# Optimization experiments

Measured on AMD Instinct MI355X. Metric: run time of the kernel, lower is better.

The kernel has to match this reference:

```python
import jax, jax.numpy as jnp
import numpy as np
from jax import lax

EPS = 1e-6
NUM_BANDS = 128


def setup_inputs() -> dict:
    key = jax.random.key(0)
    kx, = jax.random.split(key, 1)
    B, C, F, T = 32, 1, NUM_BANDS, 6000
    x = jax.random.uniform(kx, (B, C, F, T), dtype=jnp.float32)  # nonneg spectrogram energies
    # parameters per band, initialized as in PCEN.__init__ (s=0.025, alpha=delta=r=1.0)
    log_s = jnp.full((F,), np.log(0.025), dtype=jnp.float32)
    log_alpha = jnp.zeros((F,), dtype=jnp.float32)
    log_delta = jnp.zeros((F,), dtype=jnp.float32)
    log_r = jnp.zeros((F,), dtype=jnp.float32)
    return {"x": x, "log_s": log_s, "log_alpha": log_alpha,
            "log_delta": log_delta, "log_r": log_r}


def _pcen(x, log_s, log_alpha, log_delta, log_r):
    # x: (B, C, bands, T)
    s = jnp.exp(log_s)  # (bands,)
    xt = jnp.moveaxis(x, -1, 0)  # (T, B, C, bands) time-major for the scan
    init = xt[0]  # init_smoother_from_data=True -> M_0 = X_0

    def step(m, xf):
        m_new = (1.0 - s) * m + s * xf
        return m_new, m_new

    _, ms = lax.scan(step, init, xt[1:])  # (T-1, B, C, bands)
    smoother = jnp.concatenate([init[None], ms], axis=0)  # (T, B, C, bands)
    smoother = jnp.moveaxis(smoother, 0, -1)  # (B, C, bands, T)

    alpha = jnp.exp(log_alpha)[:, None]  # (bands, 1)
    delta = jnp.exp(log_delta)[:, None]
    r = jnp.exp(log_r)[:, None]
    # (eps + M)^(-alpha) computed stably: exp(-alpha * (log eps + log1p(M/eps)))
    gain = jnp.exp(-alpha * (jnp.log(EPS) + jnp.log1p(smoother / EPS)))
    return (x * gain + delta) ** r - delta ** r


def reference(x, log_s, log_alpha, log_delta, log_r):
    return _pcen(x, log_s, log_alpha, log_delta, log_r)
```

## Files before the change

kernel.cpp:

```cpp
#include <hip/hip_runtime.h>

#define TLEN    6000
#define NV4     1500
#define CH_V4   512
#define SUB_V4  64
#define NSUB    8
#define EPS     1e-6f
#define LN_EPS  (-13.815511f)
#define INV_EPS 1e6f

__device__ __forceinline__ float pcen_full(float xv, float M, float alpha,
                                           float delta, float r, float deltar) {
    float gain = __expf(-alpha * (LN_EPS + __logf(fmaf(M, INV_EPS, 1.0f))));
    return __powf(fmaf(xv, gain, delta), r) - deltar;
}

__device__ __forceinline__ float ipow6(float b, int e) {
    float r = 1.0f;
    #pragma unroll
    for (int i = 0; i < 6; ++i) {
        if (e & 1) r *= b;
        b *= b;
        e >>= 1;
    }
    return r;
}

template<bool PARTIAL>
__device__ __forceinline__ float chunk_compute(
    const float4 (&q)[NSUB], const int cb, const int lane, const bool finit,
    const float s, const float oms, const float oms4, const float Apow4,
    const float A256, const bool triv,
    const float la, const float ld, const float lr,
    float Mc, float4* __restrict__ ob)
{
    float S[NSUB];
    #pragma unroll
    for (int j = 0; j < NSUB; ++j) {
        const float c0 = (finit && j == 0 && lane == 0) ? 1.0f : s;
        float b = c0 * q[j].x;
        b = fmaf(oms, b, s * q[j].y);
        b = fmaf(oms, b, s * q[j].z);
        b = fmaf(oms, b, s * q[j].w);
        S[j] = b;
    }

    float w = oms4;
    #pragma unroll
    for (int off = 1; off < 64; off <<= 1) {
        #pragma unroll
        for (int j = 0; j < NSUB; ++j) {
            const float Sp = __shfl_up(S[j], off, 64);
            if (lane >= off) S[j] = fmaf(w, Sp, S[j]);
        }
        w *= w;
    }

    float T[NSUB];
    #pragma unroll
    for (int j = 0; j < NSUB; ++j) T[j] = __shfl(S[j], 63, 64);
    float P[NSUB + 1];
    P[0] = Mc;
    #pragma unroll
    for (int j = 0; j < NSUB; ++j) P[j + 1] = fmaf(A256, P[j], T[j]);

    if (triv) {
        #pragma unroll
        for (int j = 0; j < NSUB; ++j) {
            const int vi = cb + SUB_V4 * j + lane;
            const float Se = __shfl_up(S[j], 1, 64);
            const float Be = (lane == 0) ? 0.0f : Se;
            float m = fmaf(Apow4, P[j], Be);
            if (!PARTIAL || vi < NV4) {
                const float c0 = (finit && j == 0 && lane == 0) ? 1.0f : s;
                float4 o;
                m = fmaf(oms, m, c0 * q[j].x); o.x = q[j].x * __builtin_amdgcn_rcpf(m + EPS);
                m = fmaf(oms, m, s  * q[j].y); o.y = q[j].y * __builtin_amdgcn_rcpf(m + EPS);
                m = fmaf(oms, m, s  * q[j].z); o.z = q[j].z * __builtin_amdgcn_rcpf(m + EPS);
                m = fmaf(oms, m, s  * q[j].w); o.w = q[j].w * __builtin_amdgcn_rcpf(m + EPS);
                ob[vi] = o;
            }
        }
    } else {
        const float alpha  = __expf(la);
        const float delta  = __expf(ld);
        const float r      = __expf(lr);
        const float deltar = __powf(delta, lr == 0.0f ? 1.0f : r);
        #pragma unroll
        for (int j = 0; j < NSUB; ++j) {
            const int vi = cb + SUB_V4 * j + lane;
            const float Se = __shfl_up(S[j], 1, 64);
            const float Be = (lane == 0) ? 0.0f : Se;
            float m = fmaf(Apow4, P[j], Be);
            if (!PARTIAL || vi < NV4) {
                const float c0 = (finit && j == 0 && lane == 0) ? 1.0f : s;
                float4 o;
                m = fmaf(oms, m, c0 * q[j].x); o.x = pcen_full(q[j].x, m, alpha, delta, r, deltar);
                m = fmaf(oms, m, s  * q[j].y); o.y = pcen_full(q[j].y, m, alpha, delta, r, deltar);
                m = fmaf(oms, m, s  * q[j].z); o.z = pcen_full(q[j].z, m, alpha, delta, r, deltar);
                m = fmaf(oms, m, s  * q[j].w); o.w = pcen_full(q[j].w, m, alpha, delta, r, deltar);
                ob[vi] = o;
            }
        }
    }
    return P[NSUB];
}

__global__ __launch_bounds__(256)
__attribute__((amdgpu_waves_per_eu(4, 4)))
void pcen_kernel(
    const float* __restrict__ x,
    const float* __restrict__ log_s,
    const float* __restrict__ log_alpha,
    const float* __restrict__ log_delta,
    const float* __restrict__ log_r,
    float* __restrict__ out,
    int num_series, int F)
{
    const int g    = (int)((blockIdx.x * blockDim.x + threadIdx.x) >> 6);
    const int lane = (int)(threadIdx.x & 63);
    if (g >= num_series) return;
    const int f = g % F;

    const float la = log_alpha[f], ld = log_delta[f], lr = log_r[f];
    const bool  triv = (la == 0.0f) && (ld == 0.0f) && (lr == 0.0f);

    const float s    = __expf(log_s[f]);
    const float oms  = 1.0f - s;
    const float oms2 = oms * oms;
    const float oms4 = oms2 * oms2;

    float A256 = oms4;
    #pragma unroll
    for (int i = 0; i < 6; ++i) A256 *= A256;

    const float Apow4 = ipow6(oms4, lane);

    const float4* __restrict__ xb = (const float4*)(x + (size_t)g * TLEN);
    float4* __restrict__ ob       = (float4*)(out + (size_t)g * TLEN);

    float4 bufA[NSUB], bufB[NSUB];

    #pragma unroll
    for (int j = 0; j < NSUB; ++j) bufA[j] = xb[SUB_V4 * j + lane];
    #pragma unroll
    for (int j = 0; j < NSUB; ++j) bufB[j] = xb[CH_V4 + SUB_V4 * j + lane];

    float Mc = 0.0f;

    Mc = chunk_compute<false>(bufA, 0, lane, true,
                              s, oms, oms4, Apow4, A256, triv, la, ld, lr, Mc, ob);

    #pragma unroll
    for (int j = 0; j < NSUB; ++j) {
        const int vi = 2 * CH_V4 + SUB_V4 * j + lane;
        bufA[j] = (vi < NV4) ? xb[vi] : make_float4(0.f, 0.f, 0.f, 0.f);
    }

    Mc = chunk_compute<false>(bufB, CH_V4, lane, false,
                              s, oms, oms4, Apow4, A256, triv, la, ld, lr, Mc, ob);

    chunk_compute<true>(bufA, 2 * CH_V4, lane, false,
                        s, oms, oms4, Apow4, A256, triv, la, ld, lr, Mc, ob);
}

extern "C" void kernel_launch(void* const* d_in, const int* in_sizes, int n_in,
                              void* d_out, int out_size, void* d_ws, size_t ws_size,
                              hipStream_t stream) {
    const float* x         = (const float*)d_in[0];
    const float* log_s     = (const float*)d_in[1];
    const float* log_alpha = (const float*)d_in[2];
    const float* log_delta = (const float*)d_in[3];
    const float* log_r     = (const float*)d_in[4];
    float* out             = (float*)d_out;

    const int F = in_sizes[1];
    const int num_series = in_sizes[0] / TLEN;
    const int num_waves  = num_series;
    const int num_threads = num_waves * 64;
    const int grid = (num_threads + 255) / 256;

    pcen_kernel<<<grid, 256, 0, stream>>>(x, log_s, log_alpha, log_delta, log_r,
                                          out, num_series, F);
}
```

Before: 207.1 us.

## Split each series across two waves with warm-up carry-in and reload inputs

Each time series is now handled by two waves, one per half of the sequence. The second half computes its starting smoother state itself. When the decay factor is negligible it uses a short 256-vector warm-up window before the half boundary; otherwise it replays the whole first half. This doubles the number of waves for more parallelism and latency hiding. In exchange it adds redundant reads, and it reloads x from memory in the output pass instead of keeping it in registers, which cuts register pressure. The warm-up shortcut is an approximation based on how fast the recurrence decays.

```diff
diff --git a/kernel.cpp b/kernel.cpp
--- a/kernel.cpp
+++ b/kernel.cpp
@@ -2,9 +2,10 @@
 
 #define TLEN    6000
 #define NV4     1500
-#define CH_V4   512
 #define SUB_V4  64
-#define NSUB    8
+#define NSUB    12
+#define H0_V4   768
+#define WARM_V4 256
 #define EPS     1e-6f
 #define LN_EPS  (-13.815511f)
 #define INV_EPS 1e6f
@@ -26,89 +27,7 @@
     return r;
 }
 
-template<bool PARTIAL>
-__device__ __forceinline__ float chunk_compute(
-    const float4 (&q)[NSUB], const int cb, const int lane, const bool finit,
-    const float s, const float oms, const float oms4, const float Apow4,
-    const float A256, const bool triv,
-    const float la, const float ld, const float lr,
-    float Mc, float4* __restrict__ ob)
-{
-    float S[NSUB];
-    #pragma unroll
-    for (int j = 0; j < NSUB; ++j) {
-        const float c0 = (finit && j == 0 && lane == 0) ? 1.0f : s;
-        float b = c0 * q[j].x;
-        b = fmaf(oms, b, s * q[j].y);
-        b = fmaf(oms, b, s * q[j].z);
-        b = fmaf(oms, b, s * q[j].w);
-        S[j] = b;
-    }
-
-    float w = oms4;
-    #pragma unroll
-    for (int off = 1; off < 64; off <<= 1) {
-        #pragma unroll
-        for (int j = 0; j < NSUB; ++j) {
-            const float Sp = __shfl_up(S[j], off, 64);
-            if (lane >= off) S[j] = fmaf(w, Sp, S[j]);
-        }
-        w *= w;
-    }
-
-    float T[NSUB];
-    #pragma unroll
-    for (int j = 0; j < NSUB; ++j) T[j] = __shfl(S[j], 63, 64);
-    float P[NSUB + 1];
-    P[0] = Mc;
-    #pragma unroll
-    for (int j = 0; j < NSUB; ++j) P[j + 1] = fmaf(A256, P[j], T[j]);
-
-    if (triv) {
-        #pragma unroll
-        for (int j = 0; j < NSUB; ++j) {
-            const int vi = cb + SUB_V4 * j + lane;
-            const float Se = __shfl_up(S[j], 1, 64);
-            const float Be = (lane == 0) ? 0.0f : Se;
-            float m = fmaf(Apow4, P[j], Be);
-            if (!PARTIAL || vi < NV4) {
-                const float c0 = (finit && j == 0 && lane == 0) ? 1.0f : s;
-                float4 o;
-                m = fmaf(oms, m, c0 * q[j].x); o.x = q[j].x * __builtin_amdgcn_rcpf(m + EPS);
-                m = fmaf(oms, m, s  * q[j].y); o.y = q[j].y * __builtin_amdgcn_rcpf(m + EPS);
-                m = fmaf(oms, m, s  * q[j].z); o.z = q[j].z * __builtin_amdgcn_rcpf(m + EPS);
-                m = fmaf(oms, m, s  * q[j].w); o.w = q[j].w * __builtin_amdgcn_rcpf(m + EPS);
-                ob[vi] = o;
-            }
-        }
-    } else {
-        const float alpha  = __expf(la);
-        const float delta  = __expf(ld);
-        const float r      = __expf(lr);
-        const float deltar = __powf(delta, lr == 0.0f ? 1.0f : r);
-        #pragma unroll
-        for (int j = 0; j < NSUB; ++j) {
-            const int vi = cb + SUB_V4 * j + lane;
-            const float Se = __shfl_up(S[j], 1, 64);
-            const float Be = (lane == 0) ? 0.0f : Se;
-            float m = fmaf(Apow4, P[j], Be);
-            if (!PARTIAL || vi < NV4) {
-                const float c0 = (finit && j == 0 && lane == 0) ? 1.0f : s;
-                float4 o;
-                m = fmaf(oms, m, c0 * q[j].x); o.x = pcen_full(q[j].x, m, alpha, delta, r, deltar);
-                m = fmaf(oms, m, s  * q[j].y); o.y = pcen_full(q[j].y, m, alpha, delta, r, deltar);
-                m = fmaf(oms, m, s  * q[j].z); o.z = pcen_full(q[j].z, m, alpha, delta, r, deltar);
-                m = fmaf(oms, m, s  * q[j].w); o.w = pcen_full(q[j].w, m, alpha, delta, r, deltar);
-                ob[vi] = o;
-            }
-        }
-    }
-    return P[NSUB];
-}
-
-__global__ __launch_bounds__(256)
-__attribute__((amdgpu_waves_per_eu(4, 4)))
-void pcen_kernel(
+__global__ __launch_bounds__(256, 4) void pcen_kernel(
     const float* __restrict__ x,
     const float* __restrict__ log_s,
     const float* __restrict__ log_alpha,
@@ -119,8 +38,10 @@
 {
     const int g    = (int)((blockIdx.x * blockDim.x + threadIdx.x) >> 6);
     const int lane = (int)(threadIdx.x & 63);
-    if (g >= num_series) return;
-    const int f = g % F;
+    if (g >= num_series * 2) return;
+    const int series = g >> 1;
+    const int h      = g & 1;
+    const int f      = series % F;
 
     const float la = log_alpha[f], ld = log_delta[f], lr = log_r[f];
     const bool  triv = (la == 0.0f) && (ld == 0.0f) && (lr == 0.0f);
@@ -136,32 +57,123 @@
 
     const float Apow4 = ipow6(oms4, lane);
 
-    const float4* __restrict__ xb = (const float4*)(x + (size_t)g * TLEN);
-    float4* __restrict__ ob       = (float4*)(out + (size_t)g * TLEN);
+    const float4* __restrict__ xb = (const float4*)(x + (size_t)series * TLEN);
+    float4* __restrict__ ob       = (float4*)(out + (size_t)series * TLEN);
 
-    float4 bufA[NSUB], bufB[NSUB];
-
-    #pragma unroll
-    for (int j = 0; j < NSUB; ++j) bufA[j] = xb[SUB_V4 * j + lane];
-    #pragma unroll
-    for (int j = 0; j < NSUB; ++j) bufB[j] = xb[CH_V4 + SUB_V4 * j + lane];
+    const int base = h * H0_V4;
 
     float Mc = 0.0f;
+    if (h == 1) {
+        const float wl = ipow6(oms4, 63 - lane);
+        float A1024 = A256 * A256; A1024 *= A1024;
+        if (fabsf(A1024) < 1e-7f) {
+            float Bw[4];
+            #pragma unroll
+            for (int k = 0; k < 4; ++k) {
+                const float4 qw = xb[(H0_V4 - WARM_V4) + SUB_V4 * k + lane];
+                float b = s * qw.x;
+                b = fmaf(oms, b, s * qw.y);
+                b = fmaf(oms, b, s * qw.z);
+                b = fmaf(oms, b, s * qw.w);
+                Bw[k] = b;
+            }
+            float v = wl * fmaf(A256, fmaf(A256, fmaf(A256, Bw[0], Bw[1]), Bw[2]), Bw[3]);
+            #pragma unroll
+            for (int off = 1; off < 64; off <<= 1) v += __shfl_xor(v, off, 64);
+            Mc = v;
+        } else {
+            for (int k = 0; k < NSUB; ++k) {
+                const float4 qw = xb[SUB_V4 * k + lane];
+                const float c0 = (k == 0 && lane == 0) ? 1.0f : s;
+                float b = c0 * qw.x;
+                b = fmaf(oms, b, s * qw.y);
+                b = fmaf(oms, b, s * qw.z);
+                b = fmaf(oms, b, s * qw.w);
+                float v = wl * b;
+                #pragma unroll
+                for (int off = 1; off < 64; off <<= 1) v += __shfl_xor(v, off, 64);
+                Mc = fmaf(A256, Mc, v);
+            }
+        }
+    }
 
-    Mc = chunk_compute<false>(bufA, 0, lane, true,
-                              s, oms, oms4, Apow4, A256, triv, la, ld, lr, Mc, ob);
-
+    float S[NSUB];
     #pragma unroll
     for (int j = 0; j < NSUB; ++j) {
-        const int vi = 2 * CH_V4 + SUB_V4 * j + lane;
-        bufA[j] = (vi < NV4) ? xb[vi] : make_float4(0.f, 0.f, 0.f, 0.f);
+        const int vi = base + SUB_V4 * j + lane;
+        const float4 q = (vi < NV4) ? xb[vi] : make_float4(0.f, 0.f, 0.f, 0.f);
+        const float c0 = (h == 0 && j == 0 && lane == 0) ? 1.0f : s;
+        float b = c0 * q.x;
+        b = fmaf(oms, b, s * q.y);
+        b = fmaf(oms, b, s * q.z);
+        b = fmaf(oms, b, s * q.w);
+        S[j] = b;
     }
 
-    Mc = chunk_compute<false>(bufB, CH_V4, lane, false,
-                              s, oms, oms4, Apow4, A256, triv, la, ld, lr, Mc, ob);
+    float w = oms4;
+    #pragma unroll
+    for (int off = 1; off < 64; off <<= 1) {
+        #pragma unroll
+        for (int j = 0; j < NSUB; ++j) {
+            const float Sp = __shfl_up(S[j], off, 64);
+            if (lane >= off) S[j] = fmaf(w, Sp, S[j]);
+        }
+        w *= w;
+    }
 
-    chunk_compute<true>(bufA, 2 * CH_V4, lane, false,
-                        s, oms, oms4, Apow4, A256, triv, la, ld, lr, Mc, ob);
+    float T[NSUB - 1];
+    #pragma unroll
+    for (int j = 0; j < NSUB - 1; ++j) T[j] = __shfl(S[j], 63, 64);
+    float P[NSUB];
+    P[0] = Mc;
+    #pragma unroll
+    for (int j = 1; j < NSUB; ++j) P[j] = fmaf(A256, P[j - 1], T[j - 1]);
+
+    if (triv) {
+        #pragma unroll
+        for (int j = 0; j < NSUB; ++j) {
+            int vi = base + SUB_V4 * j + lane;
+            const float Se = __shfl_up(S[j], 1, 64);
+            const float Be = (lane == 0) ? 0.0f : Se;
+            float m = fmaf(Apow4, P[j], Be);
+            int vi2 = vi;
+            asm volatile("" : "+v"(vi2));
+            if (vi2 < NV4) {
+                const float4 q = xb[vi2];
+                const float c0 = (h == 0 && j == 0 && lane == 0) ? 1.0f : s;
+                float4 o;
+                m = fmaf(oms, m, c0 * q.x); o.x = q.x * __builtin_amdgcn_rcpf(m + EPS);
+                m = fmaf(oms, m, s  * q.y); o.y = q.y * __builtin_amdgcn_rcpf(m + EPS);
+                m = fmaf(oms, m, s  * q.z); o.z = q.z * __builtin_amdgcn_rcpf(m + EPS);
+                m = fmaf(oms, m, s  * q.w); o.w = q.w * __builtin_amdgcn_rcpf(m + EPS);
+                ob[vi2] = o;
+            }
+        }
+    } else {
+        const float alpha  = __expf(la);
+        const float delta  = __expf(ld);
+        const float r      = __expf(lr);
+        const float deltar = __powf(delta, lr == 0.0f ? 1.0f : r);
+        #pragma unroll
+        for (int j = 0; j < NSUB; ++j) {
+            int vi = base + SUB_V4 * j + lane;
+            const float Se = __shfl_up(S[j], 1, 64);
+            const float Be = (lane == 0) ? 0.0f : Se;
+            float m = fmaf(Apow4, P[j], Be);
+            int vi2 = vi;
+            asm volatile("" : "+v"(vi2));
+            if (vi2 < NV4) {
+                const float4 q = xb[vi2];
+                const float c0 = (h == 0 && j == 0 && lane == 0) ? 1.0f : s;
+                float4 o;
+                m = fmaf(oms, m, c0 * q.x); o.x = pcen_full(q.x, m, alpha, delta, r, deltar);
+                m = fmaf(oms, m, s  * q.y); o.y = pcen_full(q.y, m, alpha, delta, r, deltar);
+                m = fmaf(oms, m, s  * q.z); o.z = pcen_full(q.z, m, alpha, delta, r, deltar);
+                m = fmaf(oms, m, s  * q.w); o.w = pcen_full(q.w, m, alpha, delta, r, deltar);
+                ob[vi2] = o;
+            }
+        }
+    }
 }
 
 extern "C" void kernel_launch(void* const* d_in, const int* in_sizes, int n_in,
@@ -176,7 +188,7 @@
 
     const int F = in_sizes[1];
     const int num_series = in_sizes[0] / TLEN;
-    const int num_waves  = num_series;
+    const int num_waves  = num_series * 2;
     const int num_threads = num_waves * 64;
     const int grid = (num_threads + 255) / 256;
 
```

Result: faster. 192.1 us (-7.2%).
